# Kernel tuning notes

Measured on AMD Instinct MI355X. Metric: run time of the kernel, lower is better.

## Reference

```python
import jax, jax.numpy as jnp
import numpy as np

H = 12  # n_heads

def setup_inputs() -> dict:
    key = jax.random.key(0)
    ks = jax.random.split(key, 7)
    dim = 768
    x = jax.random.normal(ks[0], (2, 8, 4, 256, dim), dtype=jnp.float32)
    s = dim ** -0.5
    Wq = jax.random.normal(ks[1], (dim, dim), dtype=jnp.float32) * s
    bq = jax.random.normal(ks[2], (dim,), dtype=jnp.float32) * 0.01
    Wk = jax.random.normal(ks[3], (dim, dim), dtype=jnp.float32) * s
    bk = jax.random.normal(ks[4], (dim,), dtype=jnp.float32) * 0.01
    Wv = jax.random.normal(ks[5], (dim, dim), dtype=jnp.float32) * s
    bv = jax.random.normal(ks[6], (dim,), dtype=jnp.float32) * 0.01
    return {"x": x, "Wq": Wq, "bq": bq, "Wk": Wk, "bk": bk, "Wv": Wv, "bv": bv}

def _split_heads(y):
    # [b,t,l,p,(h d)] -> [b,t,l,h,p,d]
    b, t, l, p, hd = y.shape
    return y.reshape(b, t, l, p, H, hd // H).transpose(0, 1, 2, 4, 3, 5)

def reference(x, Wq, bq, Wk, bk, Wv, bv):
    dim = x.shape[-1]
    scale = (dim / H) ** -0.5
    q = _split_heads(x @ Wq.T + bq)  # [b,t,l,h,p,d]
    k = _split_heads(x @ Wk.T + bk)
    v = _split_heads(x @ Wv.T + bv)
    dots = jnp.einsum('btlhpd,btlhqd->btlhpq', q, k) * scale
    attn = jax.nn.softmax(dots, axis=-1)
    out = jnp.einsum('btlhpq,btlhqd->btlhpd', attn, v)
    # [b,t,l,h,p,d] -> [b,t,l,p,(h d)]
    b, t, l, h, p, d = out.shape
    return out.transpose(0, 1, 2, 4, 3, 5).reshape(b, t, l, p, h * d)
```

## Files before the change

kernel.cpp:

```cpp
#include <hip/hip_runtime.h>

typedef _Float16 f16;
typedef __attribute__((ext_vector_type(2))) _Float16 f16x2;
typedef __attribute__((ext_vector_type(8))) _Float16 f16x8;
typedef __attribute__((ext_vector_type(4))) float f32x4;

#define MFMA16(a,b,c) __builtin_amdgcn_mfma_f32_16x16x32_f16(a,b,c,0,0,0)

constexpr int NSEQ = 64;
constexpr int P    = 256;
constexpr int DIMF = 768;
constexpr int NH   = 12;
constexpr int DH   = 64;
constexpr int M    = NSEQ * P;
constexpr size_t XSZ = (size_t)M * DIMF;
constexpr size_t WSZ = (size_t)DIMF * DIMF;

__device__ __forceinline__ f16x8 cvt8(const float* p) {
    const float4 u = *(const float4*)p;
    const float4 w = *(const float4*)(p + 4);
    f16x2 a = __builtin_bit_cast(f16x2, __builtin_amdgcn_cvt_pkrtz(u.x, u.y));
    f16x2 b = __builtin_bit_cast(f16x2, __builtin_amdgcn_cvt_pkrtz(u.z, u.w));
    f16x2 c = __builtin_bit_cast(f16x2, __builtin_amdgcn_cvt_pkrtz(w.x, w.y));
    f16x2 d = __builtin_bit_cast(f16x2, __builtin_amdgcn_cvt_pkrtz(w.z, w.w));
    f16x8 r;
    r[0]=a[0]; r[1]=a[1]; r[2]=b[0]; r[3]=b[1];
    r[4]=c[0]; r[5]=c[1]; r[6]=d[0]; r[7]=d[1];
    return r;
}

__device__ __forceinline__ void gload16(const void* g, void* l) {
    __builtin_amdgcn_global_load_lds(
        (const __attribute__((address_space(1))) void*)g,
        (__attribute__((address_space(3))) void*)l, 16, 0, 0);
}

__global__ __launch_bounds__(256) void conv_kernel(
    const float* __restrict__ x,
    const float* __restrict__ Wq, const float* __restrict__ Wk,
    const float* __restrict__ Wv,
    f16* __restrict__ xh, f16* __restrict__ wh)
{
    const size_t i8 = ((size_t)blockIdx.x * 256 + threadIdx.x) * 8;
    if (i8 < XSZ) {
        *(f16x8*)(xh + i8) = cvt8(x + i8);
    } else {
        const size_t j = i8 - XSZ;
        const int mtx = (int)(j / WSZ);
        const size_t r = j - (size_t)mtx * WSZ;
        const float* src = (mtx == 0 ? Wq : mtx == 1 ? Wk : Wv) + r;
        *(f16x8*)(wh + j) = cvt8(src);
    }
}

__global__ __launch_bounds__(512, 1) void proj_gemm(
    const f16* __restrict__ xh, const f16* __restrict__ wh,
    const float* __restrict__ bq, const float* __restrict__ bk,
    const float* __restrict__ bv,
    f16* __restrict__ qout, f16* __restrict__ kout, f16* __restrict__ vt)
{
    __shared__ __align__(16) char smem[114688];
    const int wg = (blockIdx.x & 7) * 96 + (blockIdx.x >> 3);
    const int nt = wg % 12;
    const int mt = wg / 12;
    const int m0 = mt * 256, n0 = nt * 192;

    const int tid  = threadIdx.x;
    const int lane = tid & 63;
    const int wave = tid >> 6;
    const int lr   = lane & 15;
    const int lg   = lane >> 4;
    const int wm   = wave >> 2;
    const int wn   = wave & 3;

    const f16* srcA = xh + (size_t)(m0 + (tid >> 3)) * DIMF + ((tid & 7) ^ ((tid >> 3) & 7)) * 8;
    const f16* srcB = wh + (size_t)(n0 + (tid >> 3)) * DIMF + ((tid & 7) ^ ((tid >> 3) & 7)) * 8;
    char* dA = smem + tid * 16;
    char* dB = smem + 65536 + tid * 16;

    const int swz0 = (lg ^ (lr & 7)) * 16;
    const char* rA = smem + (wm * 64 + lr) * 128;
    const char* rB = smem + 65536 + (wn * 48 + lr) * 128;

    f32x4 acc[2][4][3];
    #pragma unroll
    for (int ah = 0; ah < 2; ++ah)
      #pragma unroll
      for (int m = 0; m < 4; ++m)
        #pragma unroll
        for (int n = 0; n < 3; ++n) acc[ah][m][n] = (f32x4){0.f,0.f,0.f,0.f};

    f16x8 a[4][2], bf[3][2];

    #define STA(H, T, B) do {                                                     \
        gload16(srcA + (size_t)((H)*128      ) * DIMF + (T)*64, dA + (B)*32768 + (H)*16384);         \
        gload16(srcA + (size_t)((H)*128 + 64 ) * DIMF + (T)*64, dA + (B)*32768 + (H)*16384 + 8192); } while (0)
    #define STB(U, T, B)                                                          \
        gload16(srcB + (size_t)((U)*64) * DIMF + (T)*64, dB + (B)*24576 + (U)*8192)

    #define RD_A(H, B) do { _Pragma("unroll")                                     \
        for (int m = 0; m < 4; ++m) {                                             \
            a[m][0] = *(const f16x8*)(rA + (B)*32768 + (H)*16384 + m*2048 + swz0);       \
            a[m][1] = *(const f16x8*)(rA + (B)*32768 + (H)*16384 + m*2048 + (swz0^64)); } } while (0)
    #define RD_BALL(B) do { _Pragma("unroll")                                     \
        for (int n = 0; n < 3; ++n) {                                             \
            bf[n][0] = *(const f16x8*)(rB + (B)*24576 + n*2048 + swz0);           \
            bf[n][1] = *(const f16x8*)(rB + (B)*24576 + n*2048 + (swz0^64)); } } while (0)

    #define CLUSTER(AH) do {                                                      \
        __builtin_amdgcn_s_setprio(1);                                            \
        _Pragma("unroll") for (int m = 0; m < 4; ++m)                             \
        _Pragma("unroll") for (int n = 0; n < 3; ++n) {                           \
            acc[AH][m][n] = MFMA16(a[m][0], bf[n][0], acc[AH][m][n]);             \
            acc[AH][m][n] = MFMA16(a[m][1], bf[n][1], acc[AH][m][n]); }           \
        __builtin_amdgcn_s_setprio(0); } while (0)

    #define BAR  __builtin_amdgcn_s_barrier()
    #define LGKM asm volatile("s_waitcnt lgkmcnt(0)" ::: "memory")
    #define SCHB __builtin_amdgcn_sched_barrier(0)

    #define TILE(T, B, ST) do {                                                   \
        BAR;                  \
        if (ST) { STA(0, (T)+1, (B)^1); STB(0, (T)+1, (B)^1); STB(1, (T)+1, (B)^1);  \
                  SCHB; asm volatile("s_waitcnt vmcnt(4)" ::: "memory"); }        \
        else    { asm volatile("s_waitcnt vmcnt(0)" ::: "memory"); }              \
        BAR;                                                  \
        SCHB;                                                                     \
        RD_A(0, B); RD_BALL(B);                                                   \
        LGKM; SCHB;                                                               \
        CLUSTER(0);                                                               \
        if (ST) { STA(1, (T)+1, (B)^1); STB(2, (T)+1, (B)^1); }                   \
        RD_A(1, B);                                                               \
        LGKM; SCHB;                                                               \
        CLUSTER(1);                                                               \
    } while (0)

    STA(0, 0, 0); STB(0, 0, 0); STB(1, 0, 0);
    STA(1, 0, 0); STB(2, 0, 0);

    for (int it = 0; it < 6; ++it) {
        TILE(2*it,     0, true);
        TILE(2*it + 1, 1, (it < 5));
    }

    __syncthreads();

    const int mat = nt >> 2;
    const int c0  = (nt & 3) * 192;
    const int h0  = (nt & 3) * 3;
    const int seq = mt;
    const float* __restrict__ bias = mat == 0 ? bq : mat == 1 ? bk : bv;
    float bb[3];
    #pragma unroll
    for (int n = 0; n < 3; ++n) bb[n] = bias[c0 + wn*48 + n*16 + lr];

    f16 (*ep)[200] = (f16 (*)[200])smem;
    #pragma unroll
    for (int hh = 0; hh < 2; ++hh) {
        #pragma unroll
        for (int m = 0; m < 4; ++m)
            #pragma unroll
            for (int n = 0; n < 3; ++n)
                #pragma unroll
                for (int i = 0; i < 4; ++i)
                    ep[wm*64 + m*16 + lg*4 + i][wn*48 + n*16 + lr] =
                        (f16)(acc[hh][m][n][i] + bb[n]);
        __syncthreads();
        if (mat < 2) {
            f16* __restrict__ dst = mat ? kout : qout;
            const int r = tid >> 2;
            #pragma unroll
            for (int s = 0; s < 6; ++s) {
                const int ch = s*4 + (tid & 3);
                const int h  = h0 + (ch >> 3);
                const int d0 = (ch & 7) * 8;
                *(f16x8*)(dst + ((size_t)(seq*NH + h)*P + hh*128 + r)*DH + d0) =
                    *(const f16x8*)&ep[r][ch*8];
            }
        } else {
            if (tid < 384) {
                const int col = tid >> 1, rg = tid & 1;
                const int h = h0 + (col >> 6), d = col & 63;
                f16* drow = vt + ((size_t)(seq*NH + h)*DH + d)*P + hh*128 + rg*64;
                #pragma unroll
                for (int u = 0; u < 8; ++u) {
                    f16x8 vv;
                    #pragma unroll
                    for (int uu = 0; uu < 8; ++uu)
                        vv[uu] = ep[rg*64 + u*8 + uu][col];
                    *(f16x8*)(drow + u*8) = vv;
                }
            }
        }
        __syncthreads();
    }
    #undef STA
    #undef STB
    #undef RD_A
    #undef RD_BALL
    #undef CLUSTER
    #undef BAR
    #undef LGKM
    #undef SCHB
    #undef TILE
}

__global__ __launch_bounds__(512) void attn_kernel(
    const f16* __restrict__ q, const f16* __restrict__ k,
    const f16* __restrict__ vt, float* __restrict__ out)
{
    __shared__ __align__(16) char kl[32768];
    __shared__ __align__(16) char vl[32768];
    __shared__ __align__(16) char pl[8][2048];

    const int n = blockIdx.x;
    const int b = (n & 7) * 192 + (n >> 3);
    const int half = b & 1;
    const int head = (b >> 1) % NH;
    const int seq  = b / (2 * NH);

    const int tid  = threadIdx.x;
    const int lane = tid & 63;
    const int wave = tid >> 6;
    const int lr   = lane & 15;
    const int lg   = lane >> 4;

    const f16* qh = q  + (size_t)(seq*NH + head)*P*DH;
    const f16* kh = k  + (size_t)(seq*NH + head)*P*DH;
    const f16* vh = vt + (size_t)(seq*NH + head)*DH*P;

    {
        const int r0 = tid >> 3, ck = tid & 7;
        const int d0 = tid >> 5, cv = tid & 31;
        #pragma unroll
        for (int it = 0; it < 4; ++it) {
            const int row = it * 64 + r0;
            gload16(kh + row * 64 + ((ck ^ (row & 7)) * 8), kl + it * 8192 + tid * 16);
            const int d = it * 16 + d0;
            gload16(vh + d * 256 + (((cv & 24) | ((cv ^ d) & 7)) * 8), vl + it * 8192 + tid * 16);
        }
    }

    const int qr0 = half * 128 + wave * 16;
    const f16x8 aq0 = *(const f16x8*)(qh + (qr0 + lr) * DH + lg * 8);
    const f16x8 aq1 = *(const f16x8*)(qh + (qr0 + lr) * DH + 32 + lg * 8);

    __syncthreads();

    f32x4 s[16];
    #pragma unroll
    for (int t = 0; t < 16; ++t) s[t] = (f32x4){0.f,0.f,0.f,0.f};
    __builtin_amdgcn_s_setprio(1);
    #pragma unroll
    for (int t = 0; t < 16; ++t) {
        const int row = t * 16 + lr;
        const f16x8 b0 = *(const f16x8*)(kl + row * 128 + ((lg ^ (row & 7)) * 16));
        const f16x8 b1 = *(const f16x8*)(kl + row * 128 + (((lg + 4) ^ (row & 7)) * 16));
        s[t] = MFMA16(aq0, b0, s[t]);
        s[t] = MFMA16(aq1, b1, s[t]);
    }
    __builtin_amdgcn_s_setprio(0);

    float mx[4] = {-1e30f, -1e30f, -1e30f, -1e30f};
    #pragma unroll
    for (int t = 0; t < 16; ++t)
        #pragma unroll
        for (int i = 0; i < 4; ++i) mx[i] = fmaxf(mx[i], s[t][i]);
    #pragma unroll
    for (int st = 1; st < 16; st <<= 1)
        #pragma unroll
        for (int i = 0; i < 4; ++i) mx[i] = fmaxf(mx[i], __shfl_xor(mx[i], st));

    const float SCL = 0.125f * 1.44269504088896f;
    float rs[4] = {0.f, 0.f, 0.f, 0.f};
    #pragma unroll
    for (int t = 0; t < 16; ++t)
        #pragma unroll
        for (int i = 0; i < 4; ++i) {
            const float e = exp2f((s[t][i] - mx[i]) * SCL);
            s[t][i] = e;
            rs[i] += e;
        }
    #pragma unroll
    for (int st = 1; st < 16; st <<= 1)
        #pragma unroll
        for (int i = 0; i < 4; ++i) rs[i] += __shfl_xor(rs[i], st);

    char* pw = pl[wave];
    f32x4 o[4];
    #pragma unroll
    for (int t = 0; t < 4; ++t) o[t] = (f32x4){0.f,0.f,0.f,0.f};

    #pragma unroll
    for (int qq = 0; qq < 4; ++qq) {
        #pragma unroll
        for (int tt = 0; tt < 4; ++tt) {
            const int t = qq * 4 + tt;
            #pragma unroll
            for (int i = 0; i < 4; ++i) {
                const int r = lg * 4 + i;
                const int klocal = tt * 16 + lr;
                *(f16*)(pw + r * 128 + ((klocal * 2) ^ ((r & 7) << 4))) = (f16)s[t][i];
            }
        }
        __builtin_amdgcn_s_setprio(1);
        #pragma unroll
        for (int kol = 0; kol < 2; ++kol) {
            const f16x8 ap = *(const f16x8*)(pw + lr * 128 + (((kol * 4 + lg) ^ (lr & 7)) * 16));
            #pragma unroll
            for (int dt = 0; dt < 4; ++dt) {
                const int row = dt * 16 + lr;
                const int ch  = qq * 8 + kol * 4 + lg;
                const f16x8 bv_ = *(const f16x8*)(vl + row * 512 + (((ch & 24) | ((ch ^ row) & 7)) * 16));
                o[dt] = MFMA16(ap, bv_, o[dt]);
            }
        }
        __builtin_amdgcn_s_setprio(0);
    }

    #pragma unroll
    for (int i = 0; i < 4; ++i) rs[i] = 1.f / rs[i];
    float* op = out + ((size_t)seq * P + qr0) * DIMF + head * DH;
    #pragma unroll
    for (int t = 0; t < 4; ++t)
        #pragma unroll
        for (int i = 0; i < 4; ++i)
            op[(lg * 4 + i) * DIMF + t * 16 + lr] = o[t][i] * rs[i];
}

extern "C" void kernel_launch(void* const* d_in, const int* in_sizes, int n_in,
                              void* d_out, int out_size, void* d_ws, size_t ws_size,
                              hipStream_t stream) {
    const float* x  = (const float*)d_in[0];
    const float* Wq = (const float*)d_in[1];
    const float* bq = (const float*)d_in[2];
    const float* Wk = (const float*)d_in[3];
    const float* bk = (const float*)d_in[4];
    const float* Wv = (const float*)d_in[5];
    const float* bv = (const float*)d_in[6];
    float* out = (float*)d_out;

    f16* xh = (f16*)d_out;
    f16* wh = xh + XSZ;

    const size_t QSZ = (size_t)M * DIMF;
    f16* q  = (f16*)d_ws;
    f16* k  = q + QSZ;
    f16* vt = k + QSZ;

    const int convThreads = (int)((XSZ + 3 * WSZ) / 8);
    conv_kernel<<<convThreads / 256, 256, 0, stream>>>(x, Wq, Wk, Wv, xh, wh);
    proj_gemm<<<dim3(768), 512, 0, stream>>>(xh, wh, bq, bk, bv, q, k, vt);
    attn_kernel<<<dim3(NSEQ * NH * 2), 512, 0, stream>>>(q, k, vt, out);
}
```

Baseline: 115.9 us.

## Halve projection GEMM M-tile to 128 rows and double the grid

```diff
diff --git a/kernel.cpp b/kernel.cpp
--- a/kernel.cpp
+++ b/kernel.cpp
@@ -53,17 +53,17 @@
     }
 }
 
-__global__ __launch_bounds__(512, 1) void proj_gemm(
+__global__ __launch_bounds__(512, 4) void proj_gemm(
     const f16* __restrict__ xh, const f16* __restrict__ wh,
     const float* __restrict__ bq, const float* __restrict__ bk,
     const float* __restrict__ bv,
     f16* __restrict__ qout, f16* __restrict__ kout, f16* __restrict__ vt)
 {
-    __shared__ __align__(16) char smem[114688];
-    const int wg = (blockIdx.x & 7) * 96 + (blockIdx.x >> 3);
+    __shared__ __align__(16) char smem[81920];
+    const int wg = (blockIdx.x & 7) * 192 + (blockIdx.x >> 3);
     const int nt = wg % 12;
     const int mt = wg / 12;
-    const int m0 = mt * 256, n0 = nt * 192;
+    const int m0 = mt * 128, n0 = nt * 192;
 
     const int tid  = threadIdx.x;
     const int lane = tid & 63;
@@ -76,43 +76,41 @@
     const f16* srcA = xh + (size_t)(m0 + (tid >> 3)) * DIMF + ((tid & 7) ^ ((tid >> 3) & 7)) * 8;
     const f16* srcB = wh + (size_t)(n0 + (tid >> 3)) * DIMF + ((tid & 7) ^ ((tid >> 3) & 7)) * 8;
     char* dA = smem + tid * 16;
-    char* dB = smem + 65536 + tid * 16;
+    char* dB = smem + 32768 + tid * 16;
 
     const int swz0 = (lg ^ (lr & 7)) * 16;
     const char* rA = smem + (wm * 64 + lr) * 128;
-    const char* rB = smem + 65536 + (wn * 48 + lr) * 128;
-
-    f32x4 acc[2][4][3];
-    #pragma unroll
-    for (int ah = 0; ah < 2; ++ah)
-      #pragma unroll
-      for (int m = 0; m < 4; ++m)
-        #pragma unroll
-        for (int n = 0; n < 3; ++n) acc[ah][m][n] = (f32x4){0.f,0.f,0.f,0.f};
+    const char* rB = smem + 32768 + (wn * 48 + lr) * 128;
+
+    f32x4 acc[4][3];
+    #pragma unroll
+    for (int m = 0; m < 4; ++m)
+        #pragma unroll
+        for (int n = 0; n < 3; ++n) acc[m][n] = (f32x4){0.f,0.f,0.f,0.f};
 
     f16x8 a[4][2], bf[3][2];
 
-    #define STA(H, T, B) do {                                                     \
-        gload16(srcA + (size_t)((H)*128      ) * DIMF + (T)*64, dA + (B)*32768 + (H)*16384);         \
-        gload16(srcA + (size_t)((H)*128 + 64 ) * DIMF + (T)*64, dA + (B)*32768 + (H)*16384 + 8192); } while (0)
+    #define STA(T, B) do {                                                        \
+        gload16(srcA + (T)*64,                       dA + (B)*16384);             \
+        gload16(srcA + (size_t)(64*DIMF) + (T)*64,   dA + (B)*16384 + 8192); } while (0)
     #define STB(U, T, B)                                                          \
         gload16(srcB + (size_t)((U)*64) * DIMF + (T)*64, dB + (B)*24576 + (U)*8192)
 
-    #define RD_A(H, B) do { _Pragma("unroll")                                     \
+    #define RD_A(B) do { _Pragma("unroll")                                        \
         for (int m = 0; m < 4; ++m) {                                             \
-            a[m][0] = *(const f16x8*)(rA + (B)*32768 + (H)*16384 + m*2048 + swz0);       \
-            a[m][1] = *(const f16x8*)(rA + (B)*32768 + (H)*16384 + m*2048 + (swz0^64)); } } while (0)
+            a[m][0] = *(const f16x8*)(rA + (B)*16384 + m*2048 + swz0);            \
+            a[m][1] = *(const f16x8*)(rA + (B)*16384 + m*2048 + (swz0^64)); } } while (0)
     #define RD_BALL(B) do { _Pragma("unroll")                                     \
         for (int n = 0; n < 3; ++n) {                                             \
             bf[n][0] = *(const f16x8*)(rB + (B)*24576 + n*2048 + swz0);           \
             bf[n][1] = *(const f16x8*)(rB + (B)*24576 + n*2048 + (swz0^64)); } } while (0)
 
-    #define CLUSTER(AH) do {                                                      \
+    #define CLUSTER() do {                                                        \
         __builtin_amdgcn_s_setprio(1);                                            \
         _Pragma("unroll") for (int m = 0; m < 4; ++m)                             \
         _Pragma("unroll") for (int n = 0; n < 3; ++n) {                           \
-            acc[AH][m][n] = MFMA16(a[m][0], bf[n][0], acc[AH][m][n]);             \
-            acc[AH][m][n] = MFMA16(a[m][1], bf[n][1], acc[AH][m][n]); }           \
+            acc[m][n] = MFMA16(a[m][0], bf[n][0], acc[m][n]);                     \
+            acc[m][n] = MFMA16(a[m][1], bf[n][1], acc[m][n]); }                   \
         __builtin_amdgcn_s_setprio(0); } while (0)
 
     #define BAR  __builtin_amdgcn_s_barrier()
@@ -121,22 +119,18 @@
 
     #define TILE(T, B, ST) do {                                                   \
         BAR;                  \
-        if (ST) { STA(0, (T)+1, (B)^1); STB(0, (T)+1, (B)^1); STB(1, (T)+1, (B)^1);  \
-                  SCHB; asm volatile("s_waitcnt vmcnt(4)" ::: "memory"); }        \
+        if (ST) { STA((T)+1, (B)^1);                                              \
+                  STB(0, (T)+1, (B)^1); STB(1, (T)+1, (B)^1); STB(2, (T)+1, (B)^1); \
+                  SCHB; asm volatile("s_waitcnt vmcnt(5)" ::: "memory"); }        \
         else    { asm volatile("s_waitcnt vmcnt(0)" ::: "memory"); }              \
         BAR;                                                  \
         SCHB;                                                                     \
-        RD_A(0, B); RD_BALL(B);                                                   \
+        RD_A(B); RD_BALL(B);                                                      \
         LGKM; SCHB;                                                               \
-        CLUSTER(0);                                                               \
-        if (ST) { STA(1, (T)+1, (B)^1); STB(2, (T)+1, (B)^1); }                   \
-        RD_A(1, B);                                                               \
-        LGKM; SCHB;                                                               \
-        CLUSTER(1);                                                               \
+        CLUSTER();                                                                \
     } while (0)
 
-    STA(0, 0, 0); STB(0, 0, 0); STB(1, 0, 0);
-    STA(1, 0, 0); STB(2, 0, 0);
+    STA(0, 0); STB(0, 0, 0); STB(1, 0, 0); STB(2, 0, 0);
 
     for (int it = 0; it < 6; ++it) {
         TILE(2*it,     0, true);
@@ -148,7 +142,8 @@
     const int mat = nt >> 2;
     const int c0  = (nt & 3) * 192;
     const int h0  = (nt & 3) * 3;
-    const int seq = mt;
+    const int seq = mt >> 1;
+    const int p0  = (mt & 1) * 128;
     const float* __restrict__ bias = mat == 0 ? bq : mat == 1 ? bk : bv;
     float bb[3];
     #pragma unroll
@@ -156,43 +151,39 @@
 
     f16 (*ep)[200] = (f16 (*)[200])smem;
     #pragma unroll
-    for (int hh = 0; hh < 2; ++hh) {
-        #pragma unroll
-        for (int m = 0; m < 4; ++m)
+    for (int m = 0; m < 4; ++m)
+        #pragma unroll
+        for (int n = 0; n < 3; ++n)
             #pragma unroll
-            for (int n = 0; n < 3; ++n)
+            for (int i = 0; i < 4; ++i)
+                ep[wm*64 + m*16 + lg*4 + i][wn*48 + n*16 + lr] =
+                    (f16)(acc[m][n][i] + bb[n]);
+    __syncthreads();
+    if (mat < 2) {
+        f16* __restrict__ dst = mat ? kout : qout;
+        const int r = tid >> 2;
+        #pragma unroll
+        for (int s = 0; s < 6; ++s) {
+            const int ch = s*4 + (tid & 3);
+            const int h  = h0 + (ch >> 3);
+            const int d0 = (ch & 7) * 8;
+            *(f16x8*)(dst + ((size_t)(seq*NH + h)*P + p0 + r)*DH + d0) =
+                *(const f16x8*)&ep[r][ch*8];
+        }
+    } else {
+        if (tid < 384) {
+            const int col = tid >> 1, rg = tid & 1;
+            const int h = h0 + (col >> 6), d = col & 63;
+            f16* drow = vt + ((size_t)(seq*NH + h)*DH + d)*P + p0 + rg*64;
+            #pragma unroll
+            for (int u = 0; u < 8; ++u) {
+                f16x8 vv;
                 #pragma unroll
-                for (int i = 0; i < 4; ++i)
-                    ep[wm*64 + m*16 + lg*4 + i][wn*48 + n*16 + lr] =
-                        (f16)(acc[hh][m][n][i] + bb[n]);
-        __syncthreads();
-        if (mat < 2) {
-            f16* __restrict__ dst = mat ? kout : qout;
-            const int r = tid >> 2;
-            #pragma unroll
-            for (int s = 0; s < 6; ++s) {
-                const int ch = s*4 + (tid & 3);
-                const int h  = h0 + (ch >> 3);
-                const int d0 = (ch & 7) * 8;
-                *(f16x8*)(dst + ((size_t)(seq*NH + h)*P + hh*128 + r)*DH + d0) =
-                    *(const f16x8*)&ep[r][ch*8];
+                for (int uu = 0; uu < 8; ++uu)
+                    vv[uu] = ep[rg*64 + u*8 + uu][col];
+                *(f16x8*)(drow + u*8) = vv;
             }
-        } else {
-            if (tid < 384) {
-                const int col = tid >> 1, rg = tid & 1;
-                const int h = h0 + (col >> 6), d = col & 63;
-                f16* drow = vt + ((size_t)(seq*NH + h)*DH + d)*P + hh*128 + rg*64;
-                #pragma unroll
-                for (int u = 0; u < 8; ++u) {
-                    f16x8 vv;
-                    #pragma unroll
-                    for (int uu = 0; uu < 8; ++uu)
-                        vv[uu] = ep[rg*64 + u*8 + uu][col];
-                    *(f16x8*)(drow + u*8) = vv;
-                }
-            }
-        }
-        __syncthreads();
+        }
     }
     #undef STA
     #undef STB
@@ -350,6 +341,6 @@
 
     const int convThreads = (int)((XSZ + 3 * WSZ) / 8);
     conv_kernel<<<convThreads / 256, 256, 0, stream>>>(x, Wq, Wk, Wv, xh, wh);
-    proj_gemm<<<dim3(768), 512, 0, stream>>>(xh, wh, bq, bk, bv, q, k, vt);
+    proj_gemm<<<dim3(1536), 512, 0, stream>>>(xh, wh, bq, bk, bv, q, k, vt);
     attn_kernel<<<dim3(NSEQ * NH * 2), 512, 0, stream>>>(q, k, vt, out);
 }
```

Measured after the change: 112.7 us (median of 2 runs). 1.03x faster.
